# Performance work log

Hardware: AMD Instinct MI355X
Metric: run time of the kernel (lower is better)

Reference implementation:

```python
import jax, jax.numpy as jnp
import numpy as np

B, S, D = 2, 2048, 2048
H, G = 16, 4
DH = D // H  # 128
KV = G * DH  # 512


def setup_inputs() -> dict:
    key = jax.random.key(0)
    ks = jax.random.split(key, 10)
    scale = 1.0 / np.sqrt(D)
    hidden_state = jax.random.normal(ks[0], (B, S, D), dtype=jnp.float32)
    # causal mask: 1 above the diagonal (positions to block), 0 elsewhere
    casual_mask = jnp.triu(jnp.ones((S, S), dtype=jnp.float32), k=1)
    padding_mask = jnp.zeros((B, S), dtype=jnp.float32)
    Wq = jax.random.normal(ks[1], (D, D), dtype=jnp.float32) * scale
    bq = jnp.zeros((D,), dtype=jnp.float32)
    Wk = jax.random.normal(ks[2], (D, KV), dtype=jnp.float32) * scale
    bk = jnp.zeros((KV,), dtype=jnp.float32)
    Wv = jax.random.normal(ks[3], (D, KV), dtype=jnp.float32) * scale
    bv = jnp.zeros((KV,), dtype=jnp.float32)
    Wo = jax.random.normal(ks[4], (D, D), dtype=jnp.float32) * scale
    bo = jnp.zeros((D,), dtype=jnp.float32)
    return {"hidden_state": hidden_state, "casual_mask": casual_mask,
            "padding_mask": padding_mask, "Wq": Wq, "bq": bq, "Wk": Wk,
            "bk": bk, "Wv": Wv, "bv": bv, "Wo": Wo, "bo": bo}


def reference(hidden_state, casual_mask, padding_mask, Wq, bq, Wk, bk, Wv, bv, Wo, bo):
    b, s, _ = hidden_state.shape
    rep = H // G  # heads per KV group
    q = (hidden_state @ Wq + bq).reshape(b, s, H, DH).transpose(0, 2, 1, 3)  # [b,H,s,dh]
    k = (hidden_state @ Wk + bk).reshape(b, s, G, DH).transpose(0, 2, 1, 3)  # [b,G,s,dh]
    v = (hidden_state @ Wv + bv).reshape(b, s, G, DH).transpose(0, 2, 1, 3)
    # expand KV heads: each group serves H//G query heads
    k = jnp.repeat(k, rep, axis=1)  # [b,H,s,dh]
    v = jnp.repeat(v, rep, axis=1)
    scores = jnp.einsum('bhqd,bhkd->bhqk', q, k) / jnp.sqrt(jnp.float32(DH))
    scores = scores + casual_mask * (-1e9)
    scores = scores + padding_mask[:, None, None, :] * (-1e9)
    attn = jax.nn.softmax(scores, axis=-1)
    out = jnp.einsum('bhqk,bhkd->bhqd', attn, v)  # [b,H,s,dh]
    out = out.transpose(0, 2, 1, 3).reshape(b, s, D)
    return out @ Wo + bo
```

## Files before the change

kernel.cpp:

```cpp
#include <hip/hip_runtime.h>
#include <math.h>

typedef unsigned short u16;
typedef __bf16 bf16_t;
typedef u16 u16x4 __attribute__((ext_vector_type(4)));
typedef u16 u16x8 __attribute__((ext_vector_type(8)));
typedef bf16_t bf16x8 __attribute__((ext_vector_type(8)));
typedef float f32x4 __attribute__((ext_vector_type(4)));

__device__ __forceinline__ float bf2f(u16 v) {
    union { unsigned u; float f; } x; x.u = ((unsigned)v) << 16; return x.f;
}
__device__ __forceinline__ u16 f2bf(float f) {
    union { float f; unsigned u; } x; x.f = f;
    unsigned u = x.u;
    return (u16)((u + 0x7fffu + ((u >> 16) & 1u)) >> 16);
}

__device__ __forceinline__ void gload16(const u16* g, u16* l) {
    __builtin_amdgcn_global_load_lds(
        (const __attribute__((address_space(1))) void*)g,
        (__attribute__((address_space(3))) void*)l,
        16, 0, 0);
}

__device__ __forceinline__ bool is_bf16_input(const unsigned* __restrict__ probe) {
    unsigned w = probe[(threadIdx.x & 63) * 32771 + 7];
    unsigned b7 = (w >> 8) & 0x7f;
    bool hit = (b7 >= 0x38) && (b7 <= 0x3f);
    return __builtin_popcountll(__ballot(hit)) >= 32;
}

__global__ __launch_bounds__(256) void convert_kernel(
    const void* __restrict__ src, u16* __restrict__ dst, int n,
    const unsigned* __restrict__ probe)
{
    bool bf = is_bf16_input(probe);
    int i = (blockIdx.x * 256 + threadIdx.x) * 8;
    if (i >= n) return;
    if (bf) {
        *(u16x8*)&dst[i] = *(const u16x8*)&((const u16*)src)[i];
    } else {
        const float* s = (const float*)src + i;
        u16x8 o;
#pragma unroll
        for (int j = 0; j < 8; j++) o[j] = f2bf(s[j]);
        *(u16x8*)&dst[i] = o;
    }
}

__global__ __launch_bounds__(256) void tconv_kernel(
    const void* __restrict__ in, u16* __restrict__ out, int R, int C,
    const unsigned* __restrict__ probe)
{
    bool bf = is_bf16_input(probe);
    __shared__ u16 t[32][33];
    int x = threadIdx.x & 31, y = threadIdx.x >> 5;
    int bx = blockIdx.x * 32, by = blockIdx.y * 32;
    if (bf) {
        const u16* s = (const u16*)in;
#pragma unroll
        for (int i = 0; i < 32; i += 8)
            t[y + i][x] = s[(size_t)(by + y + i) * C + bx + x];
    } else {
        const float* s = (const float*)in;
#pragma unroll
        for (int i = 0; i < 32; i += 8)
            t[y + i][x] = f2bf(s[(size_t)(by + y + i) * C + bx + x]);
    }
    __syncthreads();
#pragma unroll
    for (int i = 0; i < 32; i += 8)
        out[(size_t)(bx + y + i) * R + by + x] = t[x][y + i];
}

__global__ __launch_bounds__(256) void transpose_kernel(
    const u16* __restrict__ in, u16* __restrict__ out, int R, int LD)
{
    __shared__ u16 t[32][33];
    int x = threadIdx.x & 31, y = threadIdx.x >> 5;
    int bx = blockIdx.x * 32, by = blockIdx.y * 32;
#pragma unroll
    for (int i = 0; i < 32; i += 8)
        t[y + i][x] = in[(size_t)(by + y + i) * LD + bx + x];
    __syncthreads();
#pragma unroll
    for (int i = 0; i < 32; i += 8)
        out[(size_t)(bx + y + i) * R + by + x] = t[x][y + i];
}

__global__ __launch_bounds__(256) void gemm_bias_kernel(
    const u16* __restrict__ A, const u16* __restrict__ BT,
    const void* __restrict__ bias0, const void* __restrict__ bias1,
    const void* __restrict__ bias2, void* __restrict__ Cout,
    int M, int N, int K, const unsigned* __restrict__ probe,
    int out_native, float scale)
{
    __shared__ __align__(16) u16 As[128 * 32];
    __shared__ __align__(16) u16 Bs[128 * 32];
    const int tid  = threadIdx.x;
    const int lane = tid & 63, wave = tid >> 6;
    const int quad = lane >> 4, li = lane & 15;
    const int bm = blockIdx.x * 128, bn = blockIdx.y * 128;
    const int wm = (wave >> 1) * 64, wn = (wave & 1) * 64;
    const int lrow = lane >> 2;
    const int lcol = (lane & 3) * 8;

    f32x4 acc[4][4] = {};

    for (int k0 = 0; k0 < K; k0 += 32) {
#pragma unroll
        for (int j = 0; j < 2; j++) {
            int c = wave * 2 + j;
            int row = c * 16 + lrow;
            gload16(&A [(size_t)(bm + row) * K + k0 + lcol], &As[c * 16 * 32]);
            gload16(&BT[(size_t)(bn + row) * K + k0 + lcol], &Bs[c * 16 * 32]);
        }
        __syncthreads();
        bf16x8 af[4], bfr[4];
#pragma unroll
        for (int i = 0; i < 4; i++)
            af[i]  = *(const bf16x8*)&As[(wm + i * 16 + li) * 32 + quad * 8];
#pragma unroll
        for (int i = 0; i < 4; i++)
            bfr[i] = *(const bf16x8*)&Bs[(wn + i * 16 + li) * 32 + quad * 8];
#pragma unroll
        for (int mt = 0; mt < 4; mt++)
#pragma unroll
            for (int nt = 0; nt < 4; nt++)
                acc[mt][nt] = __builtin_amdgcn_mfma_f32_16x16x32_bf16(
                    af[mt], bfr[nt], acc[mt][nt], 0, 0, 0);
        __syncthreads();
    }

    const bool bf_in = is_bf16_input(probe);
    const bool out_bf = out_native ? bf_in : true;
#pragma unroll
    for (int nt = 0; nt < 4; nt++) {
        int col = bn + wn + nt * 16 + li;
        const void* bp; int bc;
        if (col < 2048)      { bp = bias0; bc = col; }
        else if (col < 2560) { bp = bias1; bc = col - 2048; }
        else                 { bp = bias2; bc = col - 2560; }
        float bb = bf_in ? bf2f(((const u16*)bp)[bc]) : ((const float*)bp)[bc];
        if (out_bf) {
            u16* C16 = (u16*)Cout;
#pragma unroll
            for (int mt = 0; mt < 4; mt++)
#pragma unroll
                for (int r = 0; r < 4; r++) {
                    int row = bm + wm + mt * 16 + quad * 4 + r;
                    C16[(size_t)row * N + col] = f2bf((acc[mt][nt][r] + bb) * scale);
                }
        } else {
            float* Cf = (float*)Cout;
#pragma unroll
            for (int mt = 0; mt < 4; mt++)
#pragma unroll
                for (int r = 0; r < 4; r++) {
                    int row = bm + wm + mt * 16 + quad * 4 + r;
                    Cf[(size_t)row * N + col] = (acc[mt][nt][r] + bb) * scale;
                }
        }
    }
}

__global__ __launch_bounds__(256) void flash_kernel(
    const u16* __restrict__ Q, const u16* __restrict__ Kg,
    const u16* __restrict__ VT, u16* __restrict__ O,
    float* __restrict__ PO, float* __restrict__ PM, float* __restrict__ PL)
{
    constexpr int S = 2048, D = 2048, DH = 128, QKSTR = 3072;
    constexpr float SCALE = 0.08838834764831845f;
    __shared__ __align__(16) u16 Ks[32 * 136];
    __shared__ __align__(16) u16 Vt[128 * 40];
    __shared__ __align__(16) u16 Pw[4][32 * 40];

    const int tid  = threadIdx.x;
    const int wave = tid >> 6, lane = tid & 63;
    const int quad = lane >> 4, li = lane & 15;
    const int uu = blockIdx.x, h = blockIdx.y, b = blockIdx.z;
    const int split = (uu >= 10) ? 1 : 0;
    const int qt = split ? (10 + ((uu - 10) >> 1)) : uu;
    const int cc = split ? ((uu - 10) & 1) : 0;
    const int tiles = qt + 1;
    const int kmid = (tiles >> 1) * 128;
    const int kstart = cc ? kmid : 0;
    const int kend = (split && !cc) ? kmid : tiles * 128;
    const int g = h >> 2;
    const int q0w = qt * 128 + wave * 32;

    const u16* Qb = Q  + (size_t)b * S * QKSTR;
    const u16* Kb = Kg + (size_t)b * S * QKSTR;
    const u16* Vg = VT + (size_t)g * DH * (2 * S) + (size_t)b * S;

    bf16x8 qf[2][4];
#pragma unroll
    for (int m = 0; m < 2; m++)
#pragma unroll
        for (int c = 0; c < 4; c++)
            qf[m][c] = *(const bf16x8*)&Qb[(size_t)(q0w + m * 16 + li) * QKSTR
                                           + h * DH + c * 32 + quad * 8];

    f32x4 oacc[2][8] = {};
    float mr[2] = { -INFINITY, -INFINITY };
    float lr[2] = { 0.f, 0.f };

    u16x8 kreg[2], vreg[2];
#pragma unroll
    for (int ch = 0; ch < 2; ch++) {
        int idx = tid + ch * 256;
        kreg[ch] = *(const u16x8*)&Kb[(size_t)(kstart + (idx >> 4)) * QKSTR
                                      + g * DH + (idx & 15) * 8];
        vreg[ch] = *(const u16x8*)&Vg[(size_t)(idx >> 2) * (2 * S)
                                      + kstart + (idx & 3) * 8];
    }

    for (int kc = kstart; kc < kend; kc += 32) {
#pragma unroll
        for (int ch = 0; ch < 2; ch++) {
            int idx = tid + ch * 256;
            *(u16x8*)&Ks[(idx >> 4) * 136 + (idx & 15) * 8] = kreg[ch];
            *(u16x8*)&Vt[(idx >> 2) * 40  + (idx & 3) * 8]  = vreg[ch];
        }
        __syncthreads();

        int kn = kc + 32;
        if (kn < kend) {
#pragma unroll
            for (int ch = 0; ch < 2; ch++) {
                int idx = tid + ch * 256;
                kreg[ch] = *(const u16x8*)&Kb[(size_t)(kn + (idx >> 4)) * QKSTR
                                              + g * DH + (idx & 15) * 8];
                vreg[ch] = *(const u16x8*)&Vg[(size_t)(idx >> 2) * (2 * S)
                                              + kn + (idx & 3) * 8];
            }
        }

        if (kc <= q0w) {
            f32x4 sacc[2][2] = {};
#pragma unroll
            for (int t = 0; t < 2; t++)
#pragma unroll
                for (int c = 0; c < 4; c++) {
                    bf16x8 kf = *(const bf16x8*)&Ks[(t * 16 + li) * 136 + c * 32 + quad * 8];
#pragma unroll
                    for (int m = 0; m < 2; m++)
                        sacc[m][t] = __builtin_amdgcn_mfma_f32_16x16x32_bf16(
                            kf, qf[m][c], sacc[m][t], 0, 0, 0);
                }

            float alpha_b[2][4];
#pragma unroll
            for (int m = 0; m < 2; m++) {
                int row = q0w + m * 16 + li;
                f32x4 s0 = sacc[m][0] * SCALE;
                f32x4 s1 = sacc[m][1] * SCALE;
#pragma unroll
                for (int r = 0; r < 4; r++) {
                    int k0 = kc + quad * 4 + r;
                    if (k0 > row)      s0[r] = -INFINITY;
                    if (k0 + 16 > row) s1[r] = -INFINITY;
                }
                float mx = fmaxf(fmaxf(fmaxf(s0[0], s0[1]), fmaxf(s0[2], s0[3])),
                                 fmaxf(fmaxf(s1[0], s1[1]), fmaxf(s1[2], s1[3])));
                mx = fmaxf(mx, __shfl_xor(mx, 16));
                mx = fmaxf(mx, __shfl_xor(mx, 32));
                float mnew = fmaxf(mr[m], mx);
                float al = __expf(mr[m] - mnew);
                mr[m] = mnew;
                f32x4 p0, p1;
                float ps = 0.f;
#pragma unroll
                for (int r = 0; r < 4; r++) {
                    p0[r] = __expf(s0[r] - mnew);
                    p1[r] = __expf(s1[r] - mnew);
                    ps += p0[r] + p1[r];
                }
                ps += __shfl_xor(ps, 16);
                ps += __shfl_xor(ps, 32);
                lr[m] = lr[m] * al + ps;
                u16x4 c0, c1;
#pragma unroll
                for (int r = 0; r < 4; r++) { c0[r] = f2bf(p0[r]); c1[r] = f2bf(p1[r]); }
                *(u16x4*)&Pw[wave][(m * 16 + li) * 40 + quad * 4]      = c0;
                *(u16x4*)&Pw[wave][(m * 16 + li) * 40 + 16 + quad * 4] = c1;
#pragma unroll
                for (int r = 0; r < 4; r++)
                    alpha_b[m][r] = __shfl(al, quad * 4 + r, 16);
            }

#pragma unroll
            for (int m = 0; m < 2; m++)
#pragma unroll
                for (int dt = 0; dt < 8; dt++)
#pragma unroll
                    for (int r = 0; r < 4; r++)
                        oacc[m][dt][r] *= alpha_b[m][r];

            asm volatile("s_waitcnt lgkmcnt(0)" ::: "memory");
            union { u16x8 u; bf16x8 bv; } pc0, pc1;
            pc0.u = *(const u16x8*)&Pw[wave][(0 * 16 + li) * 40 + quad * 8];
            pc1.u = *(const u16x8*)&Pw[wave][(1 * 16 + li) * 40 + quad * 8];
            bf16x8 pf[2] = { pc0.bv, pc1.bv };

#pragma unroll
            for (int dt = 0; dt < 8; dt++) {
                bf16x8 vf = *(const bf16x8*)&Vt[(dt * 16 + li) * 40 + quad * 8];
#pragma unroll
                for (int m = 0; m < 2; m++)
                    oacc[m][dt] = __builtin_amdgcn_mfma_f32_16x16x32_bf16(
                        pf[m], vf, oacc[m][dt], 0, 0, 0);
            }
        }
        __syncthreads();
    }

    if (!split) {
        u16* Ob = O + (size_t)b * S * D;
#pragma unroll
        for (int m = 0; m < 2; m++) {
#pragma unroll
            for (int r = 0; r < 4; r++) {
                float linv = 1.0f / __shfl(lr[m], quad * 4 + r, 16);
                int row = q0w + m * 16 + quad * 4 + r;
#pragma unroll
                for (int dt = 0; dt < 8; dt++)
                    Ob[(size_t)row * D + h * DH + dt * 16 + li] =
                        f2bf(oacc[m][dt][r] * linv);
            }
        }
    } else {
        const int gu = (b * 16 + h) * 12 + (qt - 10) * 2 + cc;
        float* POu = PO + (size_t)gu * 16384;
#pragma unroll
        for (int m = 0; m < 2; m++)
#pragma unroll
            for (int r = 0; r < 4; r++) {
                int rl = wave * 32 + m * 16 + quad * 4 + r;
#pragma unroll
                for (int dt = 0; dt < 8; dt++)
                    POu[rl * 128 + dt * 16 + li] = oacc[m][dt][r];
            }
        if (quad == 0) {
#pragma unroll
            for (int m = 0; m < 2; m++) {
                int rl = wave * 32 + m * 16 + li;
                PM[gu * 128 + rl] = mr[m];
                PL[gu * 128 + rl] = lr[m];
            }
        }
    }
}

__global__ __launch_bounds__(256) void combine_kernel(
    const float* __restrict__ PO, const float* __restrict__ PM,
    const float* __restrict__ PL, u16* __restrict__ O)
{
    constexpr int S = 2048, D = 2048;
    const int qt = 10 + blockIdx.x, h = blockIdx.y, b = blockIdx.z;
    const int g0 = (b * 16 + h) * 12 + blockIdx.x * 2;
    const int t = threadIdx.x;
    const int row = t >> 1, half = (t & 1) * 64;

    float m0 = PM[g0 * 128 + row], m1 = PM[(g0 + 1) * 128 + row];
    float l0 = PL[g0 * 128 + row], l1 = PL[(g0 + 1) * 128 + row];
    float M = fmaxf(m0, m1);
    float w0 = __expf(m0 - M), w1 = __expf(m1 - M);
    float linv = 1.0f / (l0 * w0 + l1 * w1);

    const float* p0 = PO + (size_t)g0 * 16384 + row * 128 + half;
    const float* p1 = p0 + 16384;
    u16* out = O + (size_t)(b * S + qt * 128 + row) * D + h * 128 + half;
#pragma unroll
    for (int j = 0; j < 64; j += 4) {
        f32x4 a = *(const f32x4*)&p0[j];
        f32x4 c = *(const f32x4*)&p1[j];
        u16x4 o;
#pragma unroll
        for (int e = 0; e < 4; e++) o[e] = f2bf((a[e] * w0 + c[e] * w1) * linv);
        *(u16x4*)&out[j] = o;
    }
}

extern "C" void kernel_launch(void* const* d_in, const int* in_sizes, int n_in,
                              void* d_out, int out_size, void* d_ws, size_t ws_size,
                              hipStream_t stream)
{
    const void* X  = d_in[0];
    const void* Wq = d_in[3];
    const void* bq = d_in[4];
    const void* Wk = d_in[5];
    const void* bk = d_in[6];
    const void* Wv = d_in[7];
    const void* bv = d_in[8];
    const void* Wo = d_in[9];
    const void* bo = d_in[10];
    const unsigned* probe = (const unsigned*)d_in[3];

    u16* ws    = (u16*)d_ws;
    u16* Xc    = ws;
    u16* WqkvT = Xc    + 8388608;
    u16* QKV   = WqkvT + 6291456;
    u16* VTb   = QKV   + 12582912;
    u16* Ob    = VTb   + 2097152;
    float* PO  = (float*)ws;
    float* PM  = PO + 384 * 16384;
    float* PL  = PM + 384 * 128;

    convert_kernel<<<4096, 256, 0, stream>>>(X, Xc, 8388608, probe);

    tconv_kernel<<<dim3(64, 64), 256, 0, stream>>>(Wq, WqkvT,               2048, 2048, probe);
    tconv_kernel<<<dim3(16, 64), 256, 0, stream>>>(Wk, WqkvT + 2048 * 2048, 2048, 512,  probe);
    tconv_kernel<<<dim3(16, 64), 256, 0, stream>>>(Wv, WqkvT + 2560 * 2048, 2048, 512,  probe);

    gemm_bias_kernel<<<dim3(32, 24), 256, 0, stream>>>(
        Xc, WqkvT, bq, bk, bv, QKV, 4096, 3072, 2048, probe, 0, 1.0f);

    transpose_kernel<<<dim3(16, 128), 256, 0, stream>>>(QKV + 2560, VTb, 4096, 3072);

    flash_kernel<<<dim3(22, 16, 2), 256, 0, stream>>>(
        QKV, QKV + 2048, VTb, Ob, PO, PM, PL);

    combine_kernel<<<dim3(6, 16, 2), 256, 0, stream>>>(PO, PM, PL, Ob);

    tconv_kernel<<<dim3(64, 64), 256, 0, stream>>>(Wo, WqkvT, 2048, 2048, probe);

    gemm_bias_kernel<<<dim3(32, 16), 256, 0, stream>>>(
        Ob, WqkvT, bo, bo, bo, d_out, 4096, 2048, 2048, probe, 1, 1.0f);
}
```

Baseline: 421.3 us.

## Rebalance causal flash split-K into 1/2/3-way chunks with spill into output buffer

Changes the flash-attention work decomposition so query tiles 7-13 are split into two KV chunks and tiles 14-15 into three, instead of splitting only tiles 10-15 in two. This gives 27 blocks per head, which is meant to reduce the imbalance caused by long causal rows and to fill the GPU better. The combine kernel now merges up to three partials. Partial outputs that no longer fit in the workspace are stored temporarily in the final output buffer, which is overwritten later. The cost is extra partial-output traffic and a larger combine step.

```diff
diff --git a/kernel.cpp b/kernel.cpp
--- a/kernel.cpp
+++ b/kernel.cpp
@@ -23,6 +23,8 @@
         (__attribute__((address_space(3))) void*)l,
         16, 0, 0);
 }
+
+#define POWS_UNITS 436
 
 __device__ __forceinline__ bool is_bf16_input(const unsigned* __restrict__ probe) {
     unsigned w = probe[(threadIdx.x & 63) * 32771 + 7];
@@ -168,7 +170,8 @@
 __global__ __launch_bounds__(256) void flash_kernel(
     const u16* __restrict__ Q, const u16* __restrict__ Kg,
     const u16* __restrict__ VT, u16* __restrict__ O,
-    float* __restrict__ PO, float* __restrict__ PM, float* __restrict__ PL)
+    float* __restrict__ POws, float* __restrict__ POdout,
+    float* __restrict__ PM, float* __restrict__ PL)
 {
     constexpr int S = 2048, D = 2048, DH = 128, QKSTR = 3072;
     constexpr float SCALE = 0.08838834764831845f;
@@ -180,13 +183,16 @@
     const int wave = tid >> 6, lane = tid & 63;
     const int quad = lane >> 4, li = lane & 15;
     const int uu = blockIdx.x, h = blockIdx.y, b = blockIdx.z;
-    const int split = (uu >= 10) ? 1 : 0;
-    const int qt = split ? (10 + ((uu - 10) >> 1)) : uu;
-    const int cc = split ? ((uu - 10) & 1) : 0;
-    const int tiles = qt + 1;
-    const int kmid = (tiles >> 1) * 128;
-    const int kstart = cc ? kmid : 0;
-    const int kend = (split && !cc) ? kmid : tiles * 128;
+    int qt, cc, nc;
+    if (uu < 7)       { qt = uu;                         cc = 0;          nc = 1; }
+    else if (uu < 21) { int t = uu - 7;  qt = 7 + (t >> 1);  cc = t & 1;  nc = 2; }
+    else              { int t = uu - 21; qt = 14 + t / 3;    cc = t % 3;  nc = 3; }
+    const int T = qt + 1;
+    const int tb = T / nc, trem = T % nc;
+    const int tcnt = tb + (cc < trem ? 1 : 0);
+    const int tstart = cc * tb + (cc < trem ? cc : trem);
+    const int kstart = tstart * 128;
+    const int kend   = (tstart + tcnt) * 128;
     const int g = h >> 2;
     const int q0w = qt * 128 + wave * 32;
 
@@ -316,7 +322,7 @@
         __syncthreads();
     }
 
-    if (!split) {
+    if (nc == 1) {
         u16* Ob = O + (size_t)b * S * D;
 #pragma unroll
         for (int m = 0; m < 2; m++) {
@@ -331,8 +337,11 @@
             }
         }
     } else {
-        const int gu = (b * 16 + h) * 12 + (qt - 10) * 2 + cc;
-        float* POu = PO + (size_t)gu * 16384;
+        const int pl = (qt <= 13) ? (qt - 7) * 2 + cc : 14 + (qt - 14) * 3 + cc;
+        const int pg = (b * 16 + h) * 20 + pl;
+        float* POu = (pg < POWS_UNITS)
+                   ? (POws   + (size_t)pg * 16384)
+                   : (POdout + (size_t)(pg - POWS_UNITS) * 16384);
 #pragma unroll
         for (int m = 0; m < 2; m++)
 #pragma unroll
@@ -346,39 +355,55 @@
 #pragma unroll
             for (int m = 0; m < 2; m++) {
                 int rl = wave * 32 + m * 16 + li;
-                PM[gu * 128 + rl] = mr[m];
-                PL[gu * 128 + rl] = lr[m];
+                PM[pg * 128 + rl] = mr[m];
+                PL[pg * 128 + rl] = lr[m];
             }
         }
     }
 }
 
 __global__ __launch_bounds__(256) void combine_kernel(
-    const float* __restrict__ PO, const float* __restrict__ PM,
-    const float* __restrict__ PL, u16* __restrict__ O)
+    const float* __restrict__ POws, const float* __restrict__ POdout,
+    const float* __restrict__ PM, const float* __restrict__ PL,
+    u16* __restrict__ O)
 {
     constexpr int S = 2048, D = 2048;
-    const int qt = 10 + blockIdx.x, h = blockIdx.y, b = blockIdx.z;
-    const int g0 = (b * 16 + h) * 12 + blockIdx.x * 2;
+    const int qt = 7 + blockIdx.x, h = blockIdx.y, b = blockIdx.z;
+    const int nc = (qt <= 13) ? 2 : 3;
+    const int pl0 = (qt <= 13) ? (qt - 7) * 2 : 14 + (qt - 14) * 3;
+    const int pg0 = (b * 16 + h) * 20 + pl0;
     const int t = threadIdx.x;
     const int row = t >> 1, half = (t & 1) * 64;
 
-    float m0 = PM[g0 * 128 + row], m1 = PM[(g0 + 1) * 128 + row];
-    float l0 = PL[g0 * 128 + row], l1 = PL[(g0 + 1) * 128 + row];
-    float M = fmaxf(m0, m1);
-    float w0 = __expf(m0 - M), w1 = __expf(m1 - M);
-    float linv = 1.0f / (l0 * w0 + l1 * w1);
-
-    const float* p0 = PO + (size_t)g0 * 16384 + row * 128 + half;
-    const float* p1 = p0 + 16384;
+    float m[3], l[3], w[3];
+    const float* p[3];
+    float M = -INFINITY;
+    for (int i = 0; i < nc; i++) {
+        int pg = pg0 + i;
+        m[i] = PM[pg * 128 + row];
+        l[i] = PL[pg * 128 + row];
+        M = fmaxf(M, m[i]);
+        p[i] = ((pg < POWS_UNITS)
+                ? (POws   + (size_t)pg * 16384)
+                : (POdout + (size_t)(pg - POWS_UNITS) * 16384))
+               + row * 128 + half;
+    }
+    float lsum = 0.f;
+    for (int i = 0; i < nc; i++) { w[i] = __expf(m[i] - M); lsum += w[i] * l[i]; }
+    float linv = 1.0f / lsum;
+
     u16* out = O + (size_t)(b * S + qt * 128 + row) * D + h * 128 + half;
-#pragma unroll
+#pragma unroll 4
     for (int j = 0; j < 64; j += 4) {
-        f32x4 a = *(const f32x4*)&p0[j];
-        f32x4 c = *(const f32x4*)&p1[j];
+        f32x4 acc = {};
+        for (int i = 0; i < nc; i++) {
+            f32x4 a = *(const f32x4*)&p[i][j];
+#pragma unroll
+            for (int e = 0; e < 4; e++) acc[e] += a[e] * w[i];
+        }
         u16x4 o;
 #pragma unroll
-        for (int e = 0; e < 4; e++) o[e] = f2bf((a[e] * w0 + c[e] * w1) * linv);
+        for (int e = 0; e < 4; e++) o[e] = f2bf(acc[e] * linv);
         *(u16x4*)&out[j] = o;
     }
 }
@@ -404,9 +429,10 @@
     u16* QKV   = WqkvT + 6291456;
     u16* VTb   = QKV   + 12582912;
     u16* Ob    = VTb   + 2097152;
-    float* PO  = (float*)ws;
-    float* PM  = PO + 384 * 16384;
-    float* PL  = PM + 384 * 128;
+    float* POws   = (float*)ws;
+    float* PM     = POws + (size_t)POWS_UNITS * 16384;
+    float* PL     = PM + 640 * 128;
+    float* POdout = (float*)d_out;
 
     convert_kernel<<<4096, 256, 0, stream>>>(X, Xc, 8388608, probe);
 
@@ -419,10 +445,10 @@
 
     transpose_kernel<<<dim3(16, 128), 256, 0, stream>>>(QKV + 2560, VTb, 4096, 3072);
 
-    flash_kernel<<<dim3(22, 16, 2), 256, 0, stream>>>(
-        QKV, QKV + 2048, VTb, Ob, PO, PM, PL);
-
-    combine_kernel<<<dim3(6, 16, 2), 256, 0, stream>>>(PO, PM, PL, Ob);
+    flash_kernel<<<dim3(27, 16, 2), 256, 0, stream>>>(
+        QKV, QKV + 2048, VTb, Ob, POws, POdout, PM, PL);
+
+    combine_kernel<<<dim3(9, 16, 2), 256, 0, stream>>>(POws, POdout, PM, PL, Ob);
 
     tconv_kernel<<<dim3(64, 64), 256, 0, stream>>>(Wo, WqkvT, 2048, 2048, probe);
 
```

Result: no change. 427.8 us (+1.5%).
